# Optimization experiments

Hardware: AMD Instinct MI355X
Metric: run time of the kernel (lower is better)

The kernel has to match this reference:

```python
import jax, jax.numpy as jnp
import numpy as np

B, N, DIN, D, NH, NL = 4, 256, 4, 64, 4, 2
DH = D // NH
EPS = 1e-5
SLOPE = 0.01  # torch LeakyReLU default negative_slope


def setup_inputs() -> dict:
    key = jax.random.key(0)
    ks = jax.random.split(key, 16)
    def p(k, shape, s=0.05):
        return jax.random.normal(k, shape, jnp.float32) * s
    return {
        "feature": jax.random.normal(ks[0], (B, N, N, DIN), jnp.float32),
        "W1": p(ks[1], (DIN, D)), "b1": jnp.zeros((D,), jnp.float32),
        "mw": p(ks[2], (NH, D)), "mb": jnp.zeros((NH,), jnp.float32),
        "bn_gamma": jnp.ones((D,), jnp.float32), "bn_beta": jnp.zeros((D,), jnp.float32),
        "Wq": p(ks[3], (NL, D, D)), "bq": jnp.zeros((NL, D), jnp.float32),
        "Wk": p(ks[4], (NL, D, D)), "bk": jnp.zeros((NL, D), jnp.float32),
        "Wv": p(ks[5], (NL, D, D)), "bv": jnp.zeros((NL, D), jnp.float32),
        "Wo": p(ks[6], (NL, D, D)), "bo": jnp.zeros((NL, D), jnp.float32),
        "ln1_g": jnp.ones((NL, D), jnp.float32), "ln1_b": jnp.zeros((NL, D), jnp.float32),
        "Wff1": p(ks[7], (NL, D, 2 * D)), "bff1": jnp.zeros((NL, 2 * D), jnp.float32),
        "Wff2": p(ks[8], (NL, 2 * D, D)), "bff2": jnp.zeros((NL, D), jnp.float32),
        "ln2_g": jnp.ones((NL, D), jnp.float32), "ln2_b": jnp.zeros((NL, D), jnp.float32),
    }


def _leaky(x):
    return jnp.where(x >= 0, x, SLOPE * x)


def _layer_norm(x, g, b):
    m = x.mean(axis=-1, keepdims=True)
    v = x.var(axis=-1, keepdims=True)
    return g * (x - m) / jnp.sqrt(v + EPS) + b


def reference(feature, W1, b1, mw, mb, bn_gamma, bn_beta,
              Wq, bq, Wk, bk, Wv, bv, Wo, bo, ln1_g, ln1_b,
              Wff1, bff1, Wff2, bff2, ln2_g, ln2_b):
    # linear1: (B,N,N,DIN) -> (B,N,N,D)
    feat = feature @ W1 + b1
    # per-head scalar attention score over node pairs: (NH,B,N,N)
    s = jnp.einsum('bijh,nh->nbij', feat, mw) + mb[:, None, None, None]
    w = jnp.exp(_leaky(s))
    w = w / w.sum(axis=3, keepdims=True)  # softmax-like over second node dim j
    # weighted aggregation: sum over i, then mean over heads -> (B,N,D)
    h = jnp.einsum('nbij,bijh->bjh', w, feat) / NH
    # BatchNorm1d over channels D, stats over (B,N) (training-mode, biased var)
    m = h.mean(axis=(0, 1))
    v = h.var(axis=(0, 1))
    x = bn_gamma * (h - m) / jnp.sqrt(v + EPS) + bn_beta  # (B,N,D)
    # standard post-LN TransformerEncoder, NL layers
    scale = 1.0 / np.sqrt(DH).astype(np.float32)
    for l in range(NL):
        q = (x @ Wq[l] + bq[l]).reshape(B, N, NH, DH)
        k = (x @ Wk[l] + bk[l]).reshape(B, N, NH, DH)
        vv = (x @ Wv[l] + bv[l]).reshape(B, N, NH, DH)
        a = jax.nn.softmax(jnp.einsum('bqhd,bkhd->bhqk', q, k) * scale, axis=-1)
        o = jnp.einsum('bhqk,bkhd->bqhd', a, vv).reshape(B, N, D) @ Wo[l] + bo[l]
        x = _layer_norm(x + o, ln1_g[l], ln1_b[l])
        f = jax.nn.relu(x @ Wff1[l] + bff1[l]) @ Wff2[l] + bff2[l]
        x = _layer_norm(x + f, ln2_g[l], ln2_b[l])
    return x
```

## Files before the change

kernel.cpp:

```cpp
#include <hip/hip_runtime.h>
#include <math.h>

#define B 4
#define N 256
#define DIN 4
#define D 64
#define NH 4
#define NL 2
#define DH 16

constexpr float EPS = 1e-5f;
constexpr float SLOPE = 0.01f;

__global__ void __launch_bounds__(512) k_rowsum(
    const float* __restrict__ feature, const float* __restrict__ W1,
    const float* __restrict__ b1, const float* __restrict__ mw,
    const float* __restrict__ mb, float* __restrict__ rs,
    float* __restrict__ bnacc ) {
    __shared__ float M[16];
    __shared__ float C[4];
    __shared__ float part[32];
    int t = threadIdx.x;
    int lane = t & 63, w = t >> 6;
    int cb = blockIdx.x;
    if (cb == 0 && t < 128) bnacc[t] = 0.f;
    if (t < 16) {
        int n = t >> 2, kk = t & 3;
        float s = 0.f;
        for (int d = 0; d < D; ++d) s += W1[kk * D + d] * mw[n * D + d];
        M[t] = s;
    } else if (t < 20) {
        int n = t - 16;
        float s = mb[n];
        for (int d = 0; d < D; ++d) s += b1[d] * mw[n * D + d];
        C[n] = s;
    }
    __syncthreads();

    int r = w & 3, mh = w >> 2;
    int bi = cb * 4 + r;
    const float4* fb = (const float4*)(feature) + (size_t)bi * N;
    float sn[4] = {0.f, 0.f, 0.f, 0.f};
#pragma unroll
    for (int mm = 0; mm < 2; ++mm) {
        float4 f = fb[lane + 64 * (mh * 2 + mm)];
#pragma unroll
        for (int n = 0; n < 4; ++n) {
            float s = C[n] + f.x * M[n*4+0] + f.y * M[n*4+1] + f.z * M[n*4+2] + f.w * M[n*4+3];
            s = (s >= 0.f) ? s : SLOPE * s;
            sn[n] += __expf(s);
        }
    }
#pragma unroll
    for (int n = 0; n < 4; ++n)
#pragma unroll
        for (int off = 32; off > 0; off >>= 1) sn[n] += __shfl_xor(sn[n], off);
    if (lane == 0) {
#pragma unroll
        for (int n = 0; n < 4; ++n) part[w * 4 + n] = sn[n];
    }
    __syncthreads();
    if (t < 16) {
        int rr = t >> 2, n = t & 3;
        rs[((size_t)(cb * 4 + rr)) * 4 + n] = part[rr * 4 + n] + part[(rr + 4) * 4 + n];
    }
}

__global__ void __launch_bounds__(512) k_aggregate(
    const float* __restrict__ feature, const float* __restrict__ W1,
    const float* __restrict__ b1, const float* __restrict__ mw,
    const float* __restrict__ mb, const float* __restrict__ rs,
    float* __restrict__ h, float* __restrict__ bnacc) {
    __shared__ float M[16];
    __shared__ float C[4];
    __shared__ float part[8][10];
    __shared__ float gacc[20];
    __shared__ float hs[4][D];
    int t = threadIdx.x;
    int lane = t & 63, w = t >> 6;
    int cb = blockIdx.x;
    if (t < 16) {
        int n = t >> 2, kk = t & 3;
        float s = 0.f;
        for (int d = 0; d < D; ++d) s += W1[kk * D + d] * mw[n * D + d];
        M[t] = s;
    } else if (t < 20) {
        int n = t - 16;
        float s = mb[n];
        for (int d = 0; d < D; ++d) s += b1[d] * mw[n * D + d];
        C[n] = s;
    }
    __syncthreads();

    int b = cb >> 6, j0 = (cb & 63) * 4;
    int i = t & 255, jh = t >> 8;
    const float4* fb = (const float4*)(feature) + ((size_t)(b * N + i) * N + j0 + jh * 2);
    float4 f[2];
    f[0] = fb[0];
    f[1] = fb[1];
    float4 r4 = *(const float4*)(rs + (size_t)(b * N + i) * 4);
    float rinv[4] = {1.f / r4.x, 1.f / r4.y, 1.f / r4.z, 1.f / r4.w};
    float acc[2][5];
#pragma unroll
    for (int jj = 0; jj < 2; ++jj) {
        float wbar = 0.f;
#pragma unroll
        for (int n = 0; n < 4; ++n) {
            float s = C[n] + f[jj].x * M[n*4+0] + f[jj].y * M[n*4+1] + f[jj].z * M[n*4+2] + f[jj].w * M[n*4+3];
            s = (s >= 0.f) ? s : SLOPE * s;
            wbar += __expf(s) * rinv[n];
        }
        wbar *= 0.25f;
        acc[jj][0] = wbar * f[jj].x; acc[jj][1] = wbar * f[jj].y;
        acc[jj][2] = wbar * f[jj].z; acc[jj][3] = wbar * f[jj].w;
        acc[jj][4] = wbar;
    }
#pragma unroll
    for (int jj = 0; jj < 2; ++jj)
#pragma unroll
        for (int c = 0; c < 5; ++c)
#pragma unroll
            for (int off = 32; off > 0; off >>= 1) acc[jj][c] += __shfl_xor(acc[jj][c], off);
    if (lane == 0) {
#pragma unroll
        for (int jj = 0; jj < 2; ++jj)
#pragma unroll
            for (int c = 0; c < 5; ++c) part[w][jj * 5 + c] = acc[jj][c];
    }
    __syncthreads();
    if (t < 20) {
        int jj = t / 5, c = t - jj * 5;
        int g = jj >> 1, jjl = jj & 1;
        gacc[t] = part[g*4+0][jjl*5+c] + part[g*4+1][jjl*5+c]
                + part[g*4+2][jjl*5+c] + part[g*4+3][jjl*5+c];
    }
    __syncthreads();
    if (t < 256) {
        float hv = gacc[w * 5 + 4] * b1[lane];
#pragma unroll
        for (int kk = 0; kk < 4; ++kk) hv += gacc[w * 5 + kk] * W1[kk * D + lane];
        h[((size_t)(b * N + j0 + w)) * D + lane] = hv;
        hs[w][lane] = hv;
    }
    __syncthreads();
    if (t < 64) {
        float s = hs[0][lane] + hs[1][lane] + hs[2][lane] + hs[3][lane];
        float sq = hs[0][lane]*hs[0][lane] + hs[1][lane]*hs[1][lane]
                 + hs[2][lane]*hs[2][lane] + hs[3][lane]*hs[3][lane];
        atomicAdd(bnacc + lane, s);
        atomicAdd(bnacc + D + lane, sq);
    }
}

__global__ void __launch_bounds__(256, 4) k_qkv0(
    const float* __restrict__ h, const float* __restrict__ bnacc,
    const float* __restrict__ bn_g, const float* __restrict__ bn_b,
    const float* __restrict__ Wq, const float* __restrict__ bq,
    const float* __restrict__ Wk, const float* __restrict__ bk,
    const float* __restrict__ Wv, const float* __restrict__ bv,
    float* __restrict__ x, float* __restrict__ q,
    float* __restrict__ k, float* __restrict__ v) {
    __shared__ float pp[4][192];
    int t = threadIdx.x, lane = t & 63, w = t >> 6, ch = lane;
    int b = blockIdx.x, n = blockIdx.y;
    int token = b * N + n;
    float mean = bnacc[ch] * (1.0f / (B * N));
    float var = bnacc[D + ch] * (1.0f / (B * N)) - mean * mean;
    float inv = rsqrtf(var + EPS);
    float xv = bn_g[ch] * (h[(size_t)token * D + ch] - mean) * inv + bn_b[ch];
    if (w == 0) x[(size_t)token * D + ch] = xv;
    float aq = 0.f, ak = 0.f, av = 0.f;
#pragma unroll
    for (int i = 0; i < 16; ++i) {
        int kk = w * 16 + i;
        float xx = __shfl(xv, kk);
        aq += xx * Wq[kk * D + ch];
        ak += xx * Wk[kk * D + ch];
        av += xx * Wv[kk * D + ch];
    }
    pp[w][ch] = aq; pp[w][64 + ch] = ak; pp[w][128 + ch] = av;
    __syncthreads();
    if (w < 3) {
        int o = w * 64;
        float val = pp[0][o + ch] + pp[1][o + ch] + pp[2][o + ch] + pp[3][o + ch];
        int head = ch >> 4, dh = ch & (DH - 1);
        size_t oidx = (((size_t)(b * NH + head)) * N + n) * DH + dh;
        if (w == 0) q[oidx] = val + bq[ch];
        else if (w == 1) k[oidx] = val + bk[ch];
        else v[oidx] = val + bv[ch];
    }
}

__global__ void __launch_bounds__(256, 4) k_layer(
    const float* __restrict__ q, const float* __restrict__ k,
    const float* __restrict__ v,
    const float* __restrict__ Wo, const float* __restrict__ bo,
    const float* __restrict__ ln1g, const float* __restrict__ ln1b,
    const float* __restrict__ Wff1, const float* __restrict__ bff1,
    const float* __restrict__ Wff2, const float* __restrict__ bff2,
    const float* __restrict__ ln2g, const float* __restrict__ ln2b,
    const float* __restrict__ Wqn, const float* __restrict__ bqn,
    const float* __restrict__ Wkn, const float* __restrict__ bkn,
    const float* __restrict__ Wvn, const float* __restrict__ bvn,
    float* __restrict__ qo, float* __restrict__ ko, float* __restrict__ vo,
    float* __restrict__ x) {
    __shared__ float attS[D];
    __shared__ float ppA[4][192];
    __shared__ float ppB[4][192];
    int t = threadIdx.x, lane = t & 63, w = t >> 6, ch = lane;
    int b = blockIdx.x, n = blockIdx.y;
    int token = b * N + n;
    size_t xidx = (size_t)token * D + ch;
    float xv = x[xidx];

    int bh = b * NH + w;
    const float* qp = q + ((size_t)bh * N + n) * DH;
    float4 qv[4];
#pragma unroll
    for (int c = 0; c < 4; ++c) qv[c] = ((const float4*)qp)[c];
    const float* kb = k + (size_t)bh * N * DH;
    const float* vb = v + (size_t)bh * N * DH;
    float o[DH];
#pragma unroll
    for (int d = 0; d < DH; ++d) o[d] = 0.f;
    float l = 0.f;
#pragma unroll 2
    for (int cc = 0; cc < 4; ++cc) {
        int key = cc * 64 + lane;
        const float4* kp4 = (const float4*)(kb + (size_t)key * DH);
        const float4* vp4 = (const float4*)(vb + (size_t)key * DH);
        float4 Kc[4], Vc[4];
#pragma unroll
        for (int c = 0; c < 4; ++c) { Kc[c] = kp4[c]; Vc[c] = vp4[c]; }
        float s = 0.f;
#pragma unroll
        for (int c = 0; c < 4; ++c)
            s += qv[c].x * Kc[c].x + qv[c].y * Kc[c].y +
                 qv[c].z * Kc[c].z + qv[c].w * Kc[c].w;
        float p = __expf(s * 0.25f);
        l += p;
#pragma unroll
        for (int c = 0; c < 4; ++c) {
            o[4*c+0] += p * Vc[c].x;
            o[4*c+1] += p * Vc[c].y;
            o[4*c+2] += p * Vc[c].z;
            o[4*c+3] += p * Vc[c].w;
        }
    }
#pragma unroll
    for (int off = 32; off > 0; off >>= 1) l += __shfl_xor(l, off);
#pragma unroll
    for (int d = 0; d < DH; ++d)
#pragma unroll
        for (int off = 32; off > 0; off >>= 1) o[d] += __shfl_xor(o[d], off);
    float rl = 1.f / l;
    if (lane < DH) {
        float sel = o[0];
#pragma unroll
        for (int d = 1; d < DH; ++d) if (lane == d) sel = o[d];
        attS[w * DH + lane] = sel * rl;
    }
    __syncthreads();

    {
        float acc = 0.f;
#pragma unroll
        for (int i = 0; i < 16; ++i) {
            int kk = w * 16 + i;
            acc += attS[kk] * Wo[kk * D + ch];
        }
        ppA[w][ch] = acc;
    }
    __syncthreads();
    float oo = bo[ch] + ppA[0][ch] + ppA[1][ch] + ppA[2][ch] + ppA[3][ch];
    float r = xv + oo;
    float s1 = r, sq1 = r * r;
#pragma unroll
    for (int off = 32; off > 0; off >>= 1) {
        s1 += __shfl_xor(s1, off);
        sq1 += __shfl_xor(sq1, off);
    }
    float mean1 = s1 * (1.0f / D);
    float var1 = sq1 * (1.0f / D) - mean1 * mean1;
    float x1 = ln1g[ch] * (r - mean1) * rsqrtf(var1 + EPS) + ln1b[ch];

    {
        float u = 0.f, g = 0.f;
#pragma unroll
        for (int i = 0; i < 16; ++i) {
            int kk = w * 16 + i;
            float xx = __shfl(x1, kk);
            u += xx * Wff1[kk * 2 * D + ch];
            g += xx * Wff1[kk * 2 * D + D + ch];
        }
        ppB[w][ch] = u; ppB[w][64 + ch] = g;
    }
    __syncthreads();
    float f1lo = fmaxf(bff1[ch] + ppB[0][ch] + ppB[1][ch] + ppB[2][ch] + ppB[3][ch], 0.f);
    float f1hi = fmaxf(bff1[D + ch] + ppB[0][64+ch] + ppB[1][64+ch] + ppB[2][64+ch] + ppB[3][64+ch], 0.f);

    {
        float src = (w < 2) ? f1lo : f1hi;
        int kb0 = (w & 1) * 32;
        float acc = 0.f;
#pragma unroll
        for (int i = 0; i < 32; ++i) {
            int kk = (w >> 1) * 64 + kb0 + i;
            float xx = __shfl(src, kb0 + i);
            acc += xx * Wff2[kk * D + ch];
        }
        ppA[w][ch] = acc;
    }
    __syncthreads();
    float o2 = bff2[ch] + ppA[0][ch] + ppA[1][ch] + ppA[2][ch] + ppA[3][ch];
    float r2 = x1 + o2;
    float s2 = r2, sq2 = r2 * r2;
#pragma unroll
    for (int off = 32; off > 0; off >>= 1) {
        s2 += __shfl_xor(s2, off);
        sq2 += __shfl_xor(sq2, off);
    }
    float mean2 = s2 * (1.0f / D);
    float var2 = sq2 * (1.0f / D) - mean2 * mean2;
    float xnew = ln2g[ch] * (r2 - mean2) * rsqrtf(var2 + EPS) + ln2b[ch];
    if (w == 0) x[xidx] = xnew;

    if (Wqn != nullptr) {
        float aq = 0.f, ak = 0.f, avv = 0.f;
#pragma unroll
        for (int i = 0; i < 16; ++i) {
            int kk = w * 16 + i;
            float xx = __shfl(xnew, kk);
            aq  += xx * Wqn[kk * D + ch];
            ak  += xx * Wkn[kk * D + ch];
            avv += xx * Wvn[kk * D + ch];
        }
        ppB[w][ch] = aq; ppB[w][64 + ch] = ak; ppB[w][128 + ch] = avv;
        __syncthreads();
        if (w < 3) {
            int off = w * 64;
            float val = ppB[0][off+ch] + ppB[1][off+ch] + ppB[2][off+ch] + ppB[3][off+ch];
            int head = ch >> 4, dh = ch & (DH - 1);
            size_t oidx = (((size_t)(b * NH + head)) * N + n) * DH + dh;
            if (w == 0) qo[oidx] = val + bqn[ch];
            else if (w == 1) ko[oidx] = val + bkn[ch];
            else vo[oidx] = val + bvn[ch];
        }
    }
}

extern "C" void kernel_launch(void* const* d_in, const int* in_sizes, int n_in,
                              void* d_out, int out_size, void* d_ws, size_t ws_size,
                              hipStream_t stream) {
    const float* feature = (const float*)d_in[0];
    const float* W1   = (const float*)d_in[1];
    const float* b1   = (const float*)d_in[2];
    const float* mw   = (const float*)d_in[3];
    const float* mb   = (const float*)d_in[4];
    const float* bn_g = (const float*)d_in[5];
    const float* bn_b = (const float*)d_in[6];
    const float* Wq   = (const float*)d_in[7];
    const float* bq   = (const float*)d_in[8];
    const float* Wk   = (const float*)d_in[9];
    const float* bk   = (const float*)d_in[10];
    const float* Wv   = (const float*)d_in[11];
    const float* bv   = (const float*)d_in[12];
    const float* Wo   = (const float*)d_in[13];
    const float* bo   = (const float*)d_in[14];
    const float* ln1g = (const float*)d_in[15];
    const float* ln1b = (const float*)d_in[16];
    const float* Wff1 = (const float*)d_in[17];
    const float* bff1 = (const float*)d_in[18];
    const float* Wff2 = (const float*)d_in[19];
    const float* bff2 = (const float*)d_in[20];
    const float* ln2g = (const float*)d_in[21];
    const float* ln2b = (const float*)d_in[22];

    float* ws    = (float*)d_ws;
    float* rs    = ws;
    float* bnacc = rs + B * N * NH;
    float* h     = bnacc + 128;
    float* q     = h + B * N * D;
    float* k0    = q + B * N * D;
    float* v0    = k0 + B * N * D;
    float* k1    = v0 + B * N * D;
    float* v1    = k1 + B * N * D;
    float* x     = (float*)d_out;

    k_rowsum<<<256, 512, 0, stream>>>(feature, W1, b1, mw, mb, rs, bnacc);
    k_aggregate<<<256, 512, 0, stream>>>(feature, W1, b1, mw, mb, rs, h, bnacc);
    k_qkv0<<<dim3(B, N), 256, 0, stream>>>(h, bnacc, bn_g, bn_b,
                                           Wq, bq, Wk, bk, Wv, bv, x, q, k0, v0);
    k_layer<<<dim3(B, N), 256, 0, stream>>>(q, k0, v0,
        Wo, bo, ln1g, ln1b, Wff1, bff1, Wff2, bff2, ln2g, ln2b,
        Wq + (size_t)D * D, bq + D, Wk + (size_t)D * D, bk + D,
        Wv + (size_t)D * D, bv + D, q, k1, v1, x);
    k_layer<<<dim3(B, N), 256, 0, stream>>>(q, k1, v1,
        Wo + (size_t)D * D, bo + D, ln1g + D, ln1b + D,
        Wff1 + (size_t)D * 2 * D, bff1 + 2 * D,
        Wff2 + (size_t)2 * D * D, bff2 + D, ln2g + D, ln2b + D,
        nullptr, nullptr, nullptr, nullptr, nullptr, nullptr,
        nullptr, nullptr, nullptr, x);
}
```

Baseline: 153.0 us.

## Map one token per wave in layer kernels and drop shared-memory reductions

```diff
diff --git a/kernel.cpp b/kernel.cpp
--- a/kernel.cpp
+++ b/kernel.cpp
@@ -12,41 +12,60 @@
 constexpr float EPS = 1e-5f;
 constexpr float SLOPE = 0.01f;
 
+__device__ __forceinline__ void mc_proj(
+    const float* __restrict__ W1, const float* __restrict__ b1,
+    const float* __restrict__ mw, const float* __restrict__ mb,
+    int lane, float* Mreg , float* Creg ) {
+    float w1v[4];
+#pragma unroll
+    for (int kk = 0; kk < 4; ++kk) w1v[kk] = W1[kk * D + lane];
+    float b1v = b1[lane];
+#pragma unroll
+    for (int n = 0; n < 4; ++n) {
+        float mwv = mw[n * D + lane];
+        float p0 = w1v[0] * mwv, p1 = w1v[1] * mwv;
+        float p2 = w1v[2] * mwv, p3 = w1v[3] * mwv;
+        float pc = b1v * mwv;
+#pragma unroll
+        for (int off = 32; off > 0; off >>= 1) {
+            p0 += __shfl_xor(p0, off); p1 += __shfl_xor(p1, off);
+            p2 += __shfl_xor(p2, off); p3 += __shfl_xor(p3, off);
+            pc += __shfl_xor(pc, off);
+        }
+        Mreg[n * 4 + 0] = p0; Mreg[n * 4 + 1] = p1;
+        Mreg[n * 4 + 2] = p2; Mreg[n * 4 + 3] = p3;
+        Creg[n] = pc + mb[n];
+    }
+}
+
 __global__ void __launch_bounds__(512) k_rowsum(
     const float* __restrict__ feature, const float* __restrict__ W1,
     const float* __restrict__ b1, const float* __restrict__ mw,
     const float* __restrict__ mb, float* __restrict__ rs,
     float* __restrict__ bnacc ) {
-    __shared__ float M[16];
-    __shared__ float C[4];
     __shared__ float part[32];
     int t = threadIdx.x;
     int lane = t & 63, w = t >> 6;
     int cb = blockIdx.x;
     if (cb == 0 && t < 128) bnacc[t] = 0.f;
-    if (t < 16) {
-        int n = t >> 2, kk = t & 3;
-        float s = 0.f;
-        for (int d = 0; d < D; ++d) s += W1[kk * D + d] * mw[n * D + d];
-        M[t] = s;
-    } else if (t < 20) {
-        int n = t - 16;
-        float s = mb[n];
-        for (int d = 0; d < D; ++d) s += b1[d] * mw[n * D + d];
-        C[n] = s;
-    }
-    __syncthreads();
 
     int r = w & 3, mh = w >> 2;
     int bi = cb * 4 + r;
     const float4* fb = (const float4*)(feature) + (size_t)bi * N;
+    float4 f0 = fb[lane + 64 * (mh * 2 + 0)];
+    float4 f1 = fb[lane + 64 * (mh * 2 + 1)];
+
+    float Mreg[16], Creg[4];
+    mc_proj(W1, b1, mw, mb, lane, Mreg, Creg);
+
     float sn[4] = {0.f, 0.f, 0.f, 0.f};
 #pragma unroll
     for (int mm = 0; mm < 2; ++mm) {
-        float4 f = fb[lane + 64 * (mh * 2 + mm)];
+        float4 f = (mm == 0) ? f0 : f1;
 #pragma unroll
         for (int n = 0; n < 4; ++n) {
-            float s = C[n] + f.x * M[n*4+0] + f.y * M[n*4+1] + f.z * M[n*4+2] + f.w * M[n*4+3];
+            float s = Creg[n] + f.x * Mreg[n*4+0] + f.y * Mreg[n*4+1]
+                              + f.z * Mreg[n*4+2] + f.w * Mreg[n*4+3];
             s = (s >= 0.f) ? s : SLOPE * s;
             sn[n] += __expf(s);
         }
@@ -71,26 +90,12 @@
     const float* __restrict__ b1, const float* __restrict__ mw,
     const float* __restrict__ mb, const float* __restrict__ rs,
     float* __restrict__ h, float* __restrict__ bnacc) {
-    __shared__ float M[16];
-    __shared__ float C[4];
     __shared__ float part[8][10];
     __shared__ float gacc[20];
     __shared__ float hs[4][D];
     int t = threadIdx.x;
     int lane = t & 63, w = t >> 6;
     int cb = blockIdx.x;
-    if (t < 16) {
-        int n = t >> 2, kk = t & 3;
-        float s = 0.f;
-        for (int d = 0; d < D; ++d) s += W1[kk * D + d] * mw[n * D + d];
-        M[t] = s;
-    } else if (t < 20) {
-        int n = t - 16;
-        float s = mb[n];
-        for (int d = 0; d < D; ++d) s += b1[d] * mw[n * D + d];
-        C[n] = s;
-    }
-    __syncthreads();
 
     int b = cb >> 6, j0 = (cb & 63) * 4;
     int i = t & 255, jh = t >> 8;
@@ -99,6 +104,14 @@
     f[0] = fb[0];
     f[1] = fb[1];
     float4 r4 = *(const float4*)(rs + (size_t)(b * N + i) * 4);
+
+    float Mreg[16], Creg[4];
+    mc_proj(W1, b1, mw, mb, lane, Mreg, Creg);
+    float w1v[4];
+#pragma unroll
+    for (int kk = 0; kk < 4; ++kk) w1v[kk] = W1[kk * D + lane];
+    float b1v = b1[lane];
+
     float rinv[4] = {1.f / r4.x, 1.f / r4.y, 1.f / r4.z, 1.f / r4.w};
     float acc[2][5];
 #pragma unroll
@@ -106,7 +119,8 @@
         float wbar = 0.f;
 #pragma unroll
         for (int n = 0; n < 4; ++n) {
-            float s = C[n] + f[jj].x * M[n*4+0] + f[jj].y * M[n*4+1] + f[jj].z * M[n*4+2] + f[jj].w * M[n*4+3];
+            float s = Creg[n] + f[jj].x * Mreg[n*4+0] + f[jj].y * Mreg[n*4+1]
+                              + f[jj].z * Mreg[n*4+2] + f[jj].w * Mreg[n*4+3];
             s = (s >= 0.f) ? s : SLOPE * s;
             wbar += __expf(s) * rinv[n];
         }
@@ -136,9 +150,9 @@
     }
     __syncthreads();
     if (t < 256) {
-        float hv = gacc[w * 5 + 4] * b1[lane];
-#pragma unroll
-        for (int kk = 0; kk < 4; ++kk) hv += gacc[w * 5 + kk] * W1[kk * D + lane];
+        float hv = gacc[w * 5 + 4] * b1v;
+#pragma unroll
+        for (int kk = 0; kk < 4; ++kk) hv += gacc[w * 5 + kk] * w1v[kk];
         h[((size_t)(b * N + j0 + w)) * D + lane] = hv;
         hs[w][lane] = hv;
     }
@@ -152,7 +166,7 @@
     }
 }
 
-__global__ void __launch_bounds__(256, 4) k_qkv0(
+__global__ void __launch_bounds__(256, 2) k_qkv0(
     const float* __restrict__ h, const float* __restrict__ bnacc,
     const float* __restrict__ bn_g, const float* __restrict__ bn_b,
     const float* __restrict__ Wq, const float* __restrict__ bq,
@@ -160,38 +174,55 @@
     const float* __restrict__ Wv, const float* __restrict__ bv,
     float* __restrict__ x, float* __restrict__ q,
     float* __restrict__ k, float* __restrict__ v) {
-    __shared__ float pp[4][192];
     int t = threadIdx.x, lane = t & 63, w = t >> 6, ch = lane;
-    int b = blockIdx.x, n = blockIdx.y;
-    int token = b * N + n;
+    int b = blockIdx.x, n = blockIdx.y * 4 + w;
+    size_t xi = ((size_t)(b * N + n)) * D + ch;
+
     float mean = bnacc[ch] * (1.0f / (B * N));
     float var = bnacc[D + ch] * (1.0f / (B * N)) - mean * mean;
     float inv = rsqrtf(var + EPS);
-    float xv = bn_g[ch] * (h[(size_t)token * D + ch] - mean) * inv + bn_b[ch];
-    if (w == 0) x[(size_t)token * D + ch] = xv;
-    float aq = 0.f, ak = 0.f, av = 0.f;
-#pragma unroll
-    for (int i = 0; i < 16; ++i) {
-        int kk = w * 16 + i;
+    float xv = bn_g[ch] * (h[xi] - mean) * inv + bn_b[ch];
+    x[xi] = xv;
+
+    float aq = bq[ch], ak = bk[ch], av = bv[ch];
+#pragma unroll
+    for (int kk = 0; kk < D; ++kk) {
         float xx = __shfl(xv, kk);
         aq += xx * Wq[kk * D + ch];
         ak += xx * Wk[kk * D + ch];
         av += xx * Wv[kk * D + ch];
     }
-    pp[w][ch] = aq; pp[w][64 + ch] = ak; pp[w][128 + ch] = av;
-    __syncthreads();
-    if (w < 3) {
-        int o = w * 64;
-        float val = pp[0][o + ch] + pp[1][o + ch] + pp[2][o + ch] + pp[3][o + ch];
-        int head = ch >> 4, dh = ch & (DH - 1);
-        size_t oidx = (((size_t)(b * NH + head)) * N + n) * DH + dh;
-        if (w == 0) q[oidx] = val + bq[ch];
-        else if (w == 1) k[oidx] = val + bk[ch];
-        else v[oidx] = val + bv[ch];
-    }
-}
-
-__global__ void __launch_bounds__(256, 4) k_layer(
+    int head = ch >> 4, dh = ch & (DH - 1);
+    size_t oidx = (((size_t)(b * NH + head)) * N + n) * DH + dh;
+    q[oidx] = aq; k[oidx] = ak; v[oidx] = av;
+}
+
+#define ATT_LOAD1(Kx, Vx, cc)                                                  \
+    {                                                                          \
+        const float4* kp4 = (const float4*)(kb + (size_t)((cc) * 64 + lane) * DH); \
+        const float4* vp4 = (const float4*)(vb + (size_t)((cc) * 64 + lane) * DH); \
+        _Pragma("unroll")                                                      \
+        for (int c = 0; c < 4; ++c) { Kx[c] = kp4[c]; Vx[c] = vp4[c]; }        \
+    }
+
+#define ATT_CHUNK1(Kx, Vx)                                                     \
+    {                                                                          \
+        float s = 0.f;                                                         \
+        _Pragma("unroll")                                                      \
+        for (int c = 0; c < 4; ++c)                                            \
+            s += qv[c].x * Kx[c].x + qv[c].y * Kx[c].y +                       \
+                 qv[c].z * Kx[c].z + qv[c].w * Kx[c].w;                        \
+        float p = __expf(s * 0.25f);                                           \
+        l += p;                                                                \
+        _Pragma("unroll")                                                      \
+        for (int c = 0; c < 4; ++c) {                                          \
+            o[4*c+0] += p * Vx[c].x; o[4*c+1] += p * Vx[c].y;                  \
+            o[4*c+2] += p * Vx[c].z; o[4*c+3] += p * Vx[c].w;                  \
+        }                                                                      \
+    }
+
+template <bool FUSE>
+__global__ void __launch_bounds__(256, 2) k_layer(
     const float* __restrict__ q, const float* __restrict__ k,
     const float* __restrict__ v,
     const float* __restrict__ Wo, const float* __restrict__ bo,
@@ -204,148 +235,117 @@
     const float* __restrict__ Wvn, const float* __restrict__ bvn,
     float* __restrict__ qo, float* __restrict__ ko, float* __restrict__ vo,
     float* __restrict__ x) {
-    __shared__ float attS[D];
-    __shared__ float ppA[4][192];
-    __shared__ float ppB[4][192];
     int t = threadIdx.x, lane = t & 63, w = t >> 6, ch = lane;
-    int b = blockIdx.x, n = blockIdx.y;
-    int token = b * N + n;
-    size_t xidx = (size_t)token * D + ch;
+    int b = blockIdx.x, n = blockIdx.y * 4 + w;
+    size_t xidx = ((size_t)b * N + n) * D + ch;
     float xv = x[xidx];
-
-    int bh = b * NH + w;
-    const float* qp = q + ((size_t)bh * N + n) * DH;
-    float4 qv[4];
-#pragma unroll
-    for (int c = 0; c < 4; ++c) qv[c] = ((const float4*)qp)[c];
-    const float* kb = k + (size_t)bh * N * DH;
-    const float* vb = v + (size_t)bh * N * DH;
-    float o[DH];
-#pragma unroll
-    for (int d = 0; d < DH; ++d) o[d] = 0.f;
-    float l = 0.f;
-#pragma unroll 2
-    for (int cc = 0; cc < 4; ++cc) {
-        int key = cc * 64 + lane;
-        const float4* kp4 = (const float4*)(kb + (size_t)key * DH);
-        const float4* vp4 = (const float4*)(vb + (size_t)key * DH);
-        float4 Kc[4], Vc[4];
-#pragma unroll
-        for (int c = 0; c < 4; ++c) { Kc[c] = kp4[c]; Vc[c] = vp4[c]; }
-        float s = 0.f;
-#pragma unroll
-        for (int c = 0; c < 4; ++c)
-            s += qv[c].x * Kc[c].x + qv[c].y * Kc[c].y +
-                 qv[c].z * Kc[c].z + qv[c].w * Kc[c].w;
-        float p = __expf(s * 0.25f);
-        l += p;
-#pragma unroll
-        for (int c = 0; c < 4; ++c) {
-            o[4*c+0] += p * Vc[c].x;
-            o[4*c+1] += p * Vc[c].y;
-            o[4*c+2] += p * Vc[c].z;
-            o[4*c+3] += p * Vc[c].w;
+    float bo_r = bo[ch], l1g = ln1g[ch], l1b = ln1b[ch];
+    float bf1a = bff1[ch], bf1b = bff1[D + ch];
+    float bf2_r = bff2[ch], l2g = ln2g[ch], l2b = ln2b[ch];
+    float bq_r = 0.f, bk_r = 0.f, bv_r = 0.f;
+    if (FUSE) { bq_r = bqn[ch]; bk_r = bkn[ch]; bv_r = bvn[ch]; }
+
+    float attv = 0.f;
+#pragma unroll
+    for (int h = 0; h < NH; ++h) {
+        const float* kb = k + (size_t)(b * NH + h) * N * DH;
+        const float* vb = v + (size_t)(b * NH + h) * N * DH;
+        const float4* qp = (const float4*)(q + ((size_t)(b * NH + h) * N + n) * DH);
+        float4 KA[4], VA[4], KB[4], VB[4];
+        ATT_LOAD1(KA, VA, 0);
+        ATT_LOAD1(KB, VB, 1);
+        float4 qv[4];
+#pragma unroll
+        for (int c = 0; c < 4; ++c) qv[c] = qp[c];
+        float o[DH];
+#pragma unroll
+        for (int d = 0; d < DH; ++d) o[d] = 0.f;
+        float l = 0.f;
+        ATT_CHUNK1(KA, VA);
+        ATT_LOAD1(KA, VA, 2);
+        ATT_CHUNK1(KB, VB);
+        ATT_LOAD1(KB, VB, 3);
+        ATT_CHUNK1(KA, VA);
+        ATT_CHUNK1(KB, VB);
+#pragma unroll
+        for (int off = 32; off > 0; off >>= 1) l += __shfl_xor(l, off);
+#pragma unroll
+        for (int d = 0; d < DH; ++d)
+#pragma unroll
+            for (int off = 32; off > 0; off >>= 1) o[d] += __shfl_xor(o[d], off);
+        float rl = 1.f / l;
+        if ((ch >> 4) == h) {
+            float sel = o[0];
+#pragma unroll
+            for (int d = 1; d < DH; ++d)
+                if ((ch & 15) == d) sel = o[d];
+            attv = sel * rl;
         }
     }
-#pragma unroll
-    for (int off = 32; off > 0; off >>= 1) l += __shfl_xor(l, off);
-#pragma unroll
-    for (int d = 0; d < DH; ++d)
-#pragma unroll
-        for (int off = 32; off > 0; off >>= 1) o[d] += __shfl_xor(o[d], off);
-    float rl = 1.f / l;
-    if (lane < DH) {
-        float sel = o[0];
-#pragma unroll
-        for (int d = 1; d < DH; ++d) if (lane == d) sel = o[d];
-        attS[w * DH + lane] = sel * rl;
-    }
-    __syncthreads();
-
-    {
-        float acc = 0.f;
-#pragma unroll
-        for (int i = 0; i < 16; ++i) {
-            int kk = w * 16 + i;
-            acc += attS[kk] * Wo[kk * D + ch];
-        }
-        ppA[w][ch] = acc;
-    }
-    __syncthreads();
-    float oo = bo[ch] + ppA[0][ch] + ppA[1][ch] + ppA[2][ch] + ppA[3][ch];
-    float r = xv + oo;
+
+    float a0 = bo_r, a1 = 0.f, a2 = 0.f, a3 = 0.f;
+#pragma unroll
+    for (int kk = 0; kk < D; kk += 4) {
+        a0 += __shfl(attv, kk + 0) * Wo[(kk + 0) * D + ch];
+        a1 += __shfl(attv, kk + 1) * Wo[(kk + 1) * D + ch];
+        a2 += __shfl(attv, kk + 2) * Wo[(kk + 2) * D + ch];
+        a3 += __shfl(attv, kk + 3) * Wo[(kk + 3) * D + ch];
+    }
+    float r = xv + (a0 + a1) + (a2 + a3);
+
     float s1 = r, sq1 = r * r;
 #pragma unroll
     for (int off = 32; off > 0; off >>= 1) {
         s1 += __shfl_xor(s1, off);
         sq1 += __shfl_xor(sq1, off);
     }
-    float mean1 = s1 * (1.0f / D);
-    float var1 = sq1 * (1.0f / D) - mean1 * mean1;
-    float x1 = ln1g[ch] * (r - mean1) * rsqrtf(var1 + EPS) + ln1b[ch];
-
-    {
-        float u = 0.f, g = 0.f;
-#pragma unroll
-        for (int i = 0; i < 16; ++i) {
-            int kk = w * 16 + i;
-            float xx = __shfl(x1, kk);
-            u += xx * Wff1[kk * 2 * D + ch];
-            g += xx * Wff1[kk * 2 * D + D + ch];
-        }
-        ppB[w][ch] = u; ppB[w][64 + ch] = g;
-    }
-    __syncthreads();
-    float f1lo = fmaxf(bff1[ch] + ppB[0][ch] + ppB[1][ch] + ppB[2][ch] + ppB[3][ch], 0.f);
-    float f1hi = fmaxf(bff1[D + ch] + ppB[0][64+ch] + ppB[1][64+ch] + ppB[2][64+ch] + ppB[3][64+ch], 0.f);
-
-    {
-        float src = (w < 2) ? f1lo : f1hi;
-        int kb0 = (w & 1) * 32;
-        float acc = 0.f;
-#pragma unroll
-        for (int i = 0; i < 32; ++i) {
-            int kk = (w >> 1) * 64 + kb0 + i;
-            float xx = __shfl(src, kb0 + i);
-            acc += xx * Wff2[kk * D + ch];
-        }
-        ppA[w][ch] = acc;
-    }
-    __syncthreads();
-    float o2 = bff2[ch] + ppA[0][ch] + ppA[1][ch] + ppA[2][ch] + ppA[3][ch];
+    float mean1 = s1 * (1.0f / D), var1 = sq1 * (1.0f / D) - mean1 * mean1;
+    float x1 = l1g * (r - mean1) * rsqrtf(var1 + EPS) + l1b;
+
+    float u0 = bf1a, u1 = 0.f, g0 = bf1b, g1 = 0.f;
+#pragma unroll
+    for (int kk = 0; kk < D; kk += 2) {
+        float xa = __shfl(x1, kk), xb = __shfl(x1, kk + 1);
+        u0 += xa * Wff1[kk * 2 * D + ch];
+        g0 += xa * Wff1[kk * 2 * D + D + ch];
+        u1 += xb * Wff1[(kk + 1) * 2 * D + ch];
+        g1 += xb * Wff1[(kk + 1) * 2 * D + D + ch];
+    }
+    float f1lo = fmaxf(u0 + u1, 0.f), f1hi = fmaxf(g0 + g1, 0.f);
+
+    float e0 = bf2_r, e1 = 0.f, e2 = 0.f, e3 = 0.f;
+#pragma unroll
+    for (int kk = 0; kk < D; kk += 2) {
+        e0 += __shfl(f1lo, kk) * Wff2[kk * D + ch];
+        e1 += __shfl(f1lo, kk + 1) * Wff2[(kk + 1) * D + ch];
+        e2 += __shfl(f1hi, kk) * Wff2[(D + kk) * D + ch];
+        e3 += __shfl(f1hi, kk + 1) * Wff2[(D + kk + 1) * D + ch];
+    }
+    float o2 = (e0 + e1) + (e2 + e3);
     float r2 = x1 + o2;
+
     float s2 = r2, sq2 = r2 * r2;
 #pragma unroll
     for (int off = 32; off > 0; off >>= 1) {
         s2 += __shfl_xor(s2, off);
         sq2 += __shfl_xor(sq2, off);
     }
-    float mean2 = s2 * (1.0f / D);
-    float var2 = sq2 * (1.0f / D) - mean2 * mean2;
-    float xnew = ln2g[ch] * (r2 - mean2) * rsqrtf(var2 + EPS) + ln2b[ch];
-    if (w == 0) x[xidx] = xnew;
-
-    if (Wqn != nullptr) {
-        float aq = 0.f, ak = 0.f, avv = 0.f;
-#pragma unroll
-        for (int i = 0; i < 16; ++i) {
-            int kk = w * 16 + i;
+    float mean2 = s2 * (1.0f / D), var2 = sq2 * (1.0f / D) - mean2 * mean2;
+    float xnew = l2g * (r2 - mean2) * rsqrtf(var2 + EPS) + l2b;
+    x[xidx] = xnew;
+
+    if (FUSE) {
+        float aq = bq_r, ak = bk_r, av = bv_r;
+#pragma unroll
+        for (int kk = 0; kk < D; ++kk) {
             float xx = __shfl(xnew, kk);
-            aq  += xx * Wqn[kk * D + ch];
-            ak  += xx * Wkn[kk * D + ch];
-            avv += xx * Wvn[kk * D + ch];
+            aq += xx * Wqn[kk * D + ch];
+            ak += xx * Wkn[kk * D + ch];
+            av += xx * Wvn[kk * D + ch];
         }
-        ppB[w][ch] = aq; ppB[w][64 + ch] = ak; ppB[w][128 + ch] = avv;
-        __syncthreads();
-        if (w < 3) {
-            int off = w * 64;
-            float val = ppB[0][off+ch] + ppB[1][off+ch] + ppB[2][off+ch] + ppB[3][off+ch];
-            int head = ch >> 4, dh = ch & (DH - 1);
-            size_t oidx = (((size_t)(b * NH + head)) * N + n) * DH + dh;
-            if (w == 0) qo[oidx] = val + bqn[ch];
-            else if (w == 1) ko[oidx] = val + bkn[ch];
-            else vo[oidx] = val + bvn[ch];
-        }
+        int head = ch >> 4, dh = ch & (DH - 1);
+        size_t oidx = (((size_t)(b * NH + head)) * N + n) * DH + dh;
+        qo[oidx] = aq; ko[oidx] = ak; vo[oidx] = av;
     }
 }
 
@@ -389,13 +389,13 @@
 
     k_rowsum<<<256, 512, 0, stream>>>(feature, W1, b1, mw, mb, rs, bnacc);
     k_aggregate<<<256, 512, 0, stream>>>(feature, W1, b1, mw, mb, rs, h, bnacc);
-    k_qkv0<<<dim3(B, N), 256, 0, stream>>>(h, bnacc, bn_g, bn_b,
-                                           Wq, bq, Wk, bk, Wv, bv, x, q, k0, v0);
-    k_layer<<<dim3(B, N), 256, 0, stream>>>(q, k0, v0,
+    k_qkv0<<<dim3(B, N / 4), 256, 0, stream>>>(h, bnacc, bn_g, bn_b,
+                                               Wq, bq, Wk, bk, Wv, bv, x, q, k0, v0);
+    k_layer<true><<<dim3(B, N / 4), 256, 0, stream>>>(q, k0, v0,
         Wo, bo, ln1g, ln1b, Wff1, bff1, Wff2, bff2, ln2g, ln2b,
         Wq + (size_t)D * D, bq + D, Wk + (size_t)D * D, bk + D,
         Wv + (size_t)D * D, bv + D, q, k1, v1, x);
-    k_layer<<<dim3(B, N), 256, 0, stream>>>(q, k1, v1,
+    k_layer<false><<<dim3(B, N / 4), 256, 0, stream>>>(q, k1, v1,
         Wo + (size_t)D * D, bo + D, ln1g + D, ln1b + D,
         Wff1 + (size_t)D * 2 * D, bff1 + 2 * D,
         Wff2 + (size_t)2 * D * D, bff2 + D, ln2g + D, ln2b + D,
```

Measured after the change: 158.7 us. 3.7% more time.
